# Performance work log

Measured on AMD Instinct MI355X. Metric: run time of the kernel, lower is better.

The kernel has to match this reference:

```python
import jax, jax.numpy as jnp
import numpy as np

DIMS, K_SIZE, V_SIZE = 256, 64, 64
B, T = 4, 4096


def setup_inputs() -> dict:
    key = jax.random.key(0)
    k1, k2, k3, k4 = jax.random.split(key, 4)
    # glorot-uniform-style init for the projection weights
    def glorot(k, fan_in, fan_out):
        lim = jnp.sqrt(6.0 / (fan_in + fan_out))
        return jax.random.uniform(k, (fan_in, fan_out), jnp.float32, -lim, lim)
    return {
        "inputs": jax.random.normal(k1, (B, T, DIMS), jnp.float32),
        "key_w": glorot(k2, DIMS, K_SIZE),
        "query_w": glorot(k3, DIMS, K_SIZE),
        "value_w": glorot(k4, DIMS, V_SIZE),
    }


def reference(inputs, key_w, query_w, value_w):
    # QKV projections: [B,T,D] @ [D,k] -> [B,T,k]
    keys = jnp.einsum('btd,dk->btk', inputs, key_w)
    queries = jnp.einsum('btd,dk->btk', inputs, query_w)
    values = jnp.einsum('btd,dv->btv', inputs, value_w)
    # full causal score matrix [B,T,T] (faithful to explicit triu mask)
    logits = jnp.einsum('bqk,bsk->bqs', queries, keys)
    q_idx = jnp.arange(logits.shape[1])[:, None]
    s_idx = jnp.arange(logits.shape[2])[None, :]
    causal = s_idx <= q_idx  # lower-triangular incl. diagonal
    sqrt_k = jnp.sqrt(jnp.asarray(key_w.shape[1], jnp.float32))
    masked = jnp.where(causal[None], logits, -jnp.inf)
    probs = jax.nn.softmax(masked / sqrt_k, axis=2)
    read = jnp.einsum('bqs,bsv->bqv', probs, values)
    return jnp.concatenate([inputs, read], axis=-1)  # [B,T,D+V]
```

## Files before the change

kernel.cpp:

```cpp
#include <hip/hip_runtime.h>

#define DIMS 256
#define HK 64
#define NB 4
#define NT 4096
#define BT (NB * NT)
#define SMAX 8

typedef unsigned short u16;
typedef unsigned int u32;

using f32x4  = __attribute__((ext_vector_type(4))) float;
using bf16x8 = __attribute__((ext_vector_type(8))) short;
using u32x2  = __attribute__((ext_vector_type(2))) u32;

__device__ __forceinline__ u16 f2bf(float f) {
    u32 u = __float_as_uint(f);
    u = (u + 0x7FFFu + ((u >> 16) & 1u)) >> 16;
    return (u16)u;
}
__device__ __forceinline__ u32 pack2(float a, float b) {
    return (u32)f2bf(a) | ((u32)f2bf(b) << 16);
}
__device__ __forceinline__ float bf2f(short h) {
    return __uint_as_float(((u32)(u16)h) << 16);
}
__device__ __forceinline__ bf16x8 ldb8(const u16* p) {
    return *reinterpret_cast<const bf16x8*>(p);
}
__device__ __forceinline__ u32 cvtpk(float a, float b) {
    u32 r;
    asm("v_cvt_pk_bf16_f32 %0, %1, %2" : "=v"(r) : "v"(a), "v"(b));
    return r;
}

__global__ __launch_bounds__(256) void prep_kernel(
    const float* __restrict__ x, const float* __restrict__ wk,
    const float* __restrict__ wq, const float* __restrict__ wv,
    float* __restrict__ out, u32* __restrict__ xb2, u16* __restrict__ Wt)
{
    const int stride = (int)(gridDim.x * blockDim.x);
    const int idx = (int)(blockIdx.x * blockDim.x + threadIdx.x);
    const f32x4* x4 = reinterpret_cast<const f32x4*>(x);
    f32x4* out4 = reinterpret_cast<f32x4*>(out);
    u32x2* xbv = reinterpret_cast<u32x2*>(xb2);

    for (int i = idx; i < BT * 64; i += stride) {
        f32x4 v = x4[i];
        out4[(size_t)(i >> 6) * 80 + (i & 63)] = v;
        u32x2 w;
        w.x = pack2(v[0], v[1]);
        w.y = pack2(v[2], v[3]);
        xbv[i] = w;
    }
    for (int i = idx; i < 12288; i += stride) {
        const int e0 = i * 4;
        const int m = e0 >> 14;
        const int r = e0 & 16383;
        const int col = r >> 8;
        const int k = r & 255;
        const float* w = (m == 0) ? wk : (m == 1) ? wq : wv;
        u32 w0 = pack2(w[(k + 0) * HK + col], w[(k + 1) * HK + col]);
        u32 w1 = pack2(w[(k + 2) * HK + col], w[(k + 3) * HK + col]);
        u32* p = reinterpret_cast<u32*>(Wt + e0);
        p[0] = w0; p[1] = w1;
    }
}

__global__ __launch_bounds__(64) void proj_kernel(
    const u16* __restrict__ xb, const u16* __restrict__ Wt,
    u16* __restrict__ Qb, u16* __restrict__ Kb, u16* __restrict__ Vt)
{
    const int l = (int)threadIdx.x;
    const int lo = l & 15;
    const int g = l >> 4;
    const int bid = (int)blockIdx.x;
    const int m = bid % 3;
    const int q0 = (bid / 3) * 16;

    bf16x8 a[8];
    const u16* xrow = xb + (size_t)(q0 + lo) * DIMS + g * 8;
    #pragma unroll
    for (int kf = 0; kf < 8; ++kf) a[kf] = ldb8(xrow + kf * 32);

    const u16* wb = Wt + m * (HK * DIMS);
    f32x4 acc[4];
    #pragma unroll
    for (int c = 0; c < 4; ++c) acc[c] = f32x4{0.f, 0.f, 0.f, 0.f};

    __builtin_amdgcn_s_setprio(1);
    #pragma unroll
    for (int c = 0; c < 4; ++c) {
        #pragma unroll
        for (int kf = 0; kf < 8; ++kf) {
            bf16x8 bf = ldb8(wb + (size_t)(16 * c + lo) * DIMS + kf * 32 + g * 8);
            acc[c] = __builtin_amdgcn_mfma_f32_16x16x32_bf16(a[kf], bf, acc[c], 0, 0, 0);
        }
    }
    __builtin_amdgcn_s_setprio(0);

    if (m == 2) {
        #pragma unroll
        for (int c = 0; c < 4; ++c)
            #pragma unroll
            for (int ii = 0; ii < 4; ++ii) {
                const int grow = q0 + 4 * g + ii;
                Vt[(size_t)((grow >> 12) * HK + 16 * c + lo) * NT + (grow & (NT - 1))] =
                    f2bf(acc[c][ii]);
            }
    } else {
        const float sc = (m == 1) ? 0.125f * 1.44269504f : 1.0f;
        u16* dst = (m == 1) ? Qb : Kb;
        #pragma unroll
        for (int c = 0; c < 4; ++c)
            #pragma unroll
            for (int ii = 0; ii < 4; ++ii)
                dst[(size_t)(q0 + 4 * g + ii) * HK + 16 * c + lo] = f2bf(acc[c][ii] * sc);
    }
}

template<bool MASK>
__device__ __forceinline__ void qk32(
    const u16* __restrict__ Kb_b, int s0, int q0,
    const bf16x8 (&qf)[2][2], float (&pls)[2], bf16x8 (&pa)[2],
    int lo, int g)
{
    bf16x8 kk[2][2];
    #pragma unroll
    for (int kh = 0; kh < 2; ++kh)
        #pragma unroll
        for (int kf = 0; kf < 2; ++kf)
            kk[kh][kf] = ldb8(Kb_b + (size_t)(s0 + 16 * kh + lo) * HK + kf * 32 + g * 8);

    const f32x4 c28 = f32x4{-28.f, -28.f, -28.f, -28.f};
    f32x4 sv[2][2];
    __builtin_amdgcn_s_setprio(1);
    #pragma unroll
    for (int rh = 0; rh < 2; ++rh)
        #pragma unroll
        for (int kh = 0; kh < 2; ++kh) {
            sv[rh][kh] = __builtin_amdgcn_mfma_f32_16x16x32_bf16(kk[kh][0], qf[rh][0], c28, 0, 0, 0);
            sv[rh][kh] = __builtin_amdgcn_mfma_f32_16x16x32_bf16(kk[kh][1], qf[rh][1], sv[rh][kh], 0, 0, 0);
        }
    __builtin_amdgcn_s_setprio(0);

    #pragma unroll
    for (int rh = 0; rh < 2; ++rh) {
        float p0[4], p1[4];
        #pragma unroll
        for (int ii = 0; ii < 4; ++ii) {
            float v0 = sv[rh][0][ii];
            float v1 = sv[rh][1][ii];
            if (MASK) {
                const int qr = q0 + 16 * rh + lo;
                if (s0 + 4 * g + ii > qr)      v0 = -1e30f;
                if (s0 + 16 + 4 * g + ii > qr) v1 = -1e30f;
            }
            p0[ii] = __builtin_amdgcn_exp2f(v0);
            p1[ii] = __builtin_amdgcn_exp2f(v1);
            pls[rh] += p0[ii] + p1[ii];
        }
        u32 a0 = cvtpk(p0[0], p0[1]), a1 = cvtpk(p0[2], p0[3]);
        u32 b0 = cvtpk(p1[0], p1[1]), b1 = cvtpk(p1[2], p1[3]);
        asm("v_permlane32_swap_b32 %0, %1" : "+v"(a0), "+v"(b0));
        asm("v_permlane16_swap_b32 %0, %1" : "+v"(a0), "+v"(b0));
        asm("v_permlane32_swap_b32 %0, %1" : "+v"(a1), "+v"(b1));
        asm("v_permlane16_swap_b32 %0, %1" : "+v"(a1), "+v"(b1));
        union { u32 w[4]; bf16x8 v; } u;
        u.w[0] = a0; u.w[1] = a1; u.w[2] = b0; u.w[3] = b1;
        pa[rh] = u.v;
    }
}

template<int NK, bool MASK>
__device__ __forceinline__ void body(
    const u16* __restrict__ Kb_b, const u16* __restrict__ Vb, int s0,
    const bf16x8 (&qf)[2][2], float (&pls)[2], f32x4 (&o)[2][4],
    int lo, int g, int q0)
{
    bf16x8 vf[NK][4];
    #pragma unroll
    for (int kf = 0; kf < NK; ++kf)
        #pragma unroll
        for (int c = 0; c < 4; ++c)
            vf[kf][c] = ldb8(Vb + (size_t)(16 * c + lo) * NT + s0 + kf * 32 + g * 8);

    #pragma unroll
    for (int t = 0; t < NK; ++t) {
        bf16x8 pa[2];
        qk32<MASK>(Kb_b, s0 + t * 32, q0, qf, pls, pa, lo, g);
        __builtin_amdgcn_s_setprio(1);
        #pragma unroll
        for (int rh = 0; rh < 2; ++rh)
            #pragma unroll
            for (int c = 0; c < 4; ++c)
                o[rh][c] = __builtin_amdgcn_mfma_f32_16x16x32_bf16(pa[rh], vf[t][c], o[rh][c], 0, 0, 0);
        __builtin_amdgcn_s_setprio(0);
    }
}

__global__ __launch_bounds__(64) void attn_kernel(
    const u16* __restrict__ Qb, const u16* __restrict__ Kb,
    const u16* __restrict__ Vt, u16* __restrict__ Opb, float* __restrict__ lp,
    const int S)
{
    const int l = (int)threadIdx.x;
    const int lo = l & 15;
    const int g = l >> 4;

    const int bid = (int)blockIdx.x;
    const int per = 4 * S;
    const int j = 127 - bid / per;
    const int r = bid % per;
    const int b = r / S;
    const int s = r % S;

    const int q0 = j * 32;
    const int nkv = j + 1;
    const int it0 = (s * nkv) / S;
    const int it1 = ((s + 1) * nkv) / S;

    const u16* Kb_b = Kb + (size_t)b * NT * HK;
    const u16* Vb = Vt + (size_t)b * HK * NT;

    bf16x8 qf[2][2];
    #pragma unroll
    for (int rh = 0; rh < 2; ++rh)
        #pragma unroll
        for (int kf = 0; kf < 2; ++kf)
            qf[rh][kf] = ldb8(Qb + (size_t)(b * NT + q0 + 16 * rh + lo) * HK + kf * 32 + g * 8);

    f32x4 o[2][4];
    float pls[2] = {0.f, 0.f};
    #pragma unroll
    for (int rh = 0; rh < 2; ++rh)
        #pragma unroll
        for (int c = 0; c < 4; ++c) o[rh][c] = f32x4{0.f, 0.f, 0.f, 0.f};

    int it = it0;
    const int itE = (s == S - 1) ? it1 - 1 : it1;
    for (; it + 1 < itE; it += 2)
        body<2, false>(Kb_b, Vb, it * 32, qf, pls, o, lo, g, q0);
    if (it < itE)
        body<1, false>(Kb_b, Vb, it * 32, qf, pls, o, lo, g, q0);
    if (s == S - 1)
        body<1, true>(Kb_b, Vb, (nkv - 1) * 32, qf, pls, o, lo, g, q0);

    const size_t rowbase = (size_t)s * BT + (size_t)b * NT + q0;
    #pragma unroll
    for (int rh = 0; rh < 2; ++rh) {
        #pragma unroll
        for (int c = 0; c < 4; ++c)
            #pragma unroll
            for (int ii = 0; ii < 4; ++ii)
                Opb[(rowbase + 16 * rh + 4 * g + ii) * HK + 16 * c + lo] = f2bf(o[rh][c][ii]);
        float sum = pls[rh];
        sum += __shfl_xor(sum, 16);
        sum += __shfl_xor(sum, 32);
        if (l < 16) lp[rowbase + 16 * rh + lo] = sum;
    }
}

__global__ __launch_bounds__(256) void merge_kernel(
    const u16* __restrict__ Opb, const float* __restrict__ lp,
    float* __restrict__ out, const int S)
{
    const int idx = (int)(blockIdx.x * 256 + threadIdx.x);
    const int row = idx >> 3;
    const int c8 = (idx & 7) * 8;

    float li = 0.f;
    for (int s = 0; s < S; ++s) li += lp[(size_t)s * BT + row];

    float acc[8];
    #pragma unroll
    for (int k = 0; k < 8; ++k) acc[k] = 0.f;
    for (int s = 0; s < S; ++s) {
        bf16x8 v = ldb8(Opb + ((size_t)s * BT + row) * HK + c8);
        #pragma unroll
        for (int k = 0; k < 8; ++k) acc[k] += bf2f(v[k]);
    }
    const float inv = 1.0f / li;
    f32x4 r0 = f32x4{acc[0] * inv, acc[1] * inv, acc[2] * inv, acc[3] * inv};
    f32x4 r1 = f32x4{acc[4] * inv, acc[5] * inv, acc[6] * inv, acc[7] * inv};
    f32x4* dst = reinterpret_cast<f32x4*>(out + (size_t)row * 320 + 256 + c8);
    dst[0] = r0;
    dst[1] = r1;
}

extern "C" void kernel_launch(void* const* d_in, const int* in_sizes, int n_in,
                              void* d_out, int out_size, void* d_ws, size_t ws_size,
                              hipStream_t stream) {
    (void)in_sizes; (void)n_in; (void)out_size;
    const float* x  = (const float*)d_in[0];
    const float* wk = (const float*)d_in[1];
    const float* wq = (const float*)d_in[2];
    const float* wv = (const float*)d_in[3];
    float* out = (float*)d_out;

    char* ws = (char*)d_ws;
    u16* Qb  = (u16*)(ws);
    u16* Kb  = (u16*)(ws + ((size_t)2  << 20));
    u16* Vt  = (u16*)(ws + ((size_t)4  << 20));
    u32* xb2 = (u32*)(ws + ((size_t)6  << 20));
    u16* xb  = (u16*)xb2;
    u16* Wt  = (u16*)(ws + ((size_t)14 << 20));
    float* lp = (float*)(ws + ((size_t)15 << 20));
    u16* Opb = (u16*)(ws + ((size_t)16 << 20));

    int S = SMAX;
    while (S > 1 && ((size_t)16 << 20) + (size_t)S * BT * HK * 2 > ws_size) S >>= 1;

    prep_kernel<<<1024, 256, 0, stream>>>(x, wk, wq, wv, out, xb2, Wt);
    proj_kernel<<<3072, 64, 0, stream>>>(xb, Wt, Qb, Kb, Vt);
    attn_kernel<<<128 * 4 * S, 64, 0, stream>>>(Qb, Kb, Vt, Opb, lp, S);
    merge_kernel<<<512, 256, 0, stream>>>(Opb, lp, out, S);
}
```

Baseline: 76.05 us.

## Fuse input conversion and passthrough copy into projection kernel

The bf16 conversion of the inputs and the copy of the inputs into the output move out of the prep kernel into the projection kernel, so the bf16 copy of x is no longer written to and read back from workspace. Each projection block now converts its 16 rows once and computes all three Q/K/V projections, where before a separate block handled each projection. The prep kernel now only transposes and converts the weights. In exchange the projection grid drops to a third as many blocks, each doing more serial work, which lowers parallelism in that stage.

```diff
diff --git a/kernel.cpp b/kernel.cpp
--- a/kernel.cpp
+++ b/kernel.cpp
@@ -5,14 +5,12 @@
 #define NB 4
 #define NT 4096
 #define BT (NB * NT)
-#define SMAX 8
 
 typedef unsigned short u16;
 typedef unsigned int u32;
 
 using f32x4  = __attribute__((ext_vector_type(4))) float;
 using bf16x8 = __attribute__((ext_vector_type(8))) short;
-using u32x2  = __attribute__((ext_vector_type(2))) u32;
 
 __device__ __forceinline__ u16 f2bf(float f) {
     u32 u = __float_as_uint(f);
@@ -33,89 +31,91 @@
     asm("v_cvt_pk_bf16_f32 %0, %1, %2" : "=v"(r) : "v"(a), "v"(b));
     return r;
 }
+__device__ __forceinline__ bf16x8 cvt8(const float* p) {
+    f32x4 a = *reinterpret_cast<const f32x4*>(p);
+    f32x4 b = *reinterpret_cast<const f32x4*>(p + 4);
+    union { u32 w[4]; bf16x8 v; } u;
+    u.w[0] = pack2(a[0], a[1]); u.w[1] = pack2(a[2], a[3]);
+    u.w[2] = pack2(b[0], b[1]); u.w[3] = pack2(b[2], b[3]);
+    return u.v;
+}
 
 __global__ __launch_bounds__(256) void prep_kernel(
-    const float* __restrict__ x, const float* __restrict__ wk,
-    const float* __restrict__ wq, const float* __restrict__ wv,
-    float* __restrict__ out, u32* __restrict__ xb2, u16* __restrict__ Wt)
-{
-    const int stride = (int)(gridDim.x * blockDim.x);
-    const int idx = (int)(blockIdx.x * blockDim.x + threadIdx.x);
-    const f32x4* x4 = reinterpret_cast<const f32x4*>(x);
-    f32x4* out4 = reinterpret_cast<f32x4*>(out);
-    u32x2* xbv = reinterpret_cast<u32x2*>(xb2);
-
-    for (int i = idx; i < BT * 64; i += stride) {
-        f32x4 v = x4[i];
-        out4[(size_t)(i >> 6) * 80 + (i & 63)] = v;
-        u32x2 w;
-        w.x = pack2(v[0], v[1]);
-        w.y = pack2(v[2], v[3]);
-        xbv[i] = w;
-    }
-    for (int i = idx; i < 12288; i += stride) {
-        const int e0 = i * 4;
-        const int m = e0 >> 14;
-        const int r = e0 & 16383;
-        const int col = r >> 8;
-        const int k = r & 255;
-        const float* w = (m == 0) ? wk : (m == 1) ? wq : wv;
-        u32 w0 = pack2(w[(k + 0) * HK + col], w[(k + 1) * HK + col]);
-        u32 w1 = pack2(w[(k + 2) * HK + col], w[(k + 3) * HK + col]);
-        u32* p = reinterpret_cast<u32*>(Wt + e0);
-        p[0] = w0; p[1] = w1;
-    }
+    const float* __restrict__ wk, const float* __restrict__ wq,
+    const float* __restrict__ wv, u16* __restrict__ Wt)
+{
+    const int i = (int)(blockIdx.x * 256 + threadIdx.x);
+    const int e0 = i * 4;
+    const int m = e0 >> 14;
+    const int r = e0 & 16383;
+    const int col = r >> 8;
+    const int k = r & 255;
+    const float* w = (m == 0) ? wk : (m == 1) ? wq : wv;
+    u32 w0 = pack2(w[(k + 0) * HK + col], w[(k + 1) * HK + col]);
+    u32 w1 = pack2(w[(k + 2) * HK + col], w[(k + 3) * HK + col]);
+    u32* p = reinterpret_cast<u32*>(Wt + e0);
+    p[0] = w0; p[1] = w1;
 }
 
 __global__ __launch_bounds__(64) void proj_kernel(
-    const u16* __restrict__ xb, const u16* __restrict__ Wt,
+    const float* __restrict__ x, const u16* __restrict__ Wt,
+    float* __restrict__ out,
     u16* __restrict__ Qb, u16* __restrict__ Kb, u16* __restrict__ Vt)
 {
     const int l = (int)threadIdx.x;
     const int lo = l & 15;
     const int g = l >> 4;
-    const int bid = (int)blockIdx.x;
-    const int m = bid % 3;
-    const int q0 = (bid / 3) * 16;
+    const int q0 = (int)blockIdx.x * 16;
+
+    const f32x4* x4 = reinterpret_cast<const f32x4*>(x);
+    f32x4* out4 = reinterpret_cast<f32x4*>(out);
+    #pragma unroll
+    for (int c = 0; c < 16; ++c) {
+        f32x4 v = x4[(size_t)(q0 + c) * 64 + l];
+        out4[(size_t)(q0 + c) * 80 + l] = v;
+    }
 
     bf16x8 a[8];
-    const u16* xrow = xb + (size_t)(q0 + lo) * DIMS + g * 8;
-    #pragma unroll
-    for (int kf = 0; kf < 8; ++kf) a[kf] = ldb8(xrow + kf * 32);
-
-    const u16* wb = Wt + m * (HK * DIMS);
-    f32x4 acc[4];
-    #pragma unroll
-    for (int c = 0; c < 4; ++c) acc[c] = f32x4{0.f, 0.f, 0.f, 0.f};
-
-    __builtin_amdgcn_s_setprio(1);
-    #pragma unroll
-    for (int c = 0; c < 4; ++c) {
-        #pragma unroll
-        for (int kf = 0; kf < 8; ++kf) {
-            bf16x8 bf = ldb8(wb + (size_t)(16 * c + lo) * DIMS + kf * 32 + g * 8);
-            acc[c] = __builtin_amdgcn_mfma_f32_16x16x32_bf16(a[kf], bf, acc[c], 0, 0, 0);
+    #pragma unroll
+    for (int kf = 0; kf < 8; ++kf)
+        a[kf] = cvt8(x + (size_t)(q0 + lo) * DIMS + kf * 32 + g * 8);
+
+    #pragma unroll
+    for (int m = 0; m < 3; ++m) {
+        const u16* wb = Wt + m * (HK * DIMS);
+        f32x4 acc[4];
+        #pragma unroll
+        for (int c = 0; c < 4; ++c) acc[c] = f32x4{0.f, 0.f, 0.f, 0.f};
+
+        __builtin_amdgcn_s_setprio(1);
+        #pragma unroll
+        for (int c = 0; c < 4; ++c) {
+            #pragma unroll
+            for (int kf = 0; kf < 8; ++kf) {
+                bf16x8 bf = ldb8(wb + (size_t)(16 * c + lo) * DIMS + kf * 32 + g * 8);
+                acc[c] = __builtin_amdgcn_mfma_f32_16x16x32_bf16(a[kf], bf, acc[c], 0, 0, 0);
+            }
         }
-    }
-    __builtin_amdgcn_s_setprio(0);
-
-    if (m == 2) {
-        #pragma unroll
-        for (int c = 0; c < 4; ++c)
-            #pragma unroll
-            for (int ii = 0; ii < 4; ++ii) {
-                const int grow = q0 + 4 * g + ii;
-                Vt[(size_t)((grow >> 12) * HK + 16 * c + lo) * NT + (grow & (NT - 1))] =
-                    f2bf(acc[c][ii]);
-            }
-    } else {
-        const float sc = (m == 1) ? 0.125f * 1.44269504f : 1.0f;
-        u16* dst = (m == 1) ? Qb : Kb;
-        #pragma unroll
-        for (int c = 0; c < 4; ++c)
-            #pragma unroll
-            for (int ii = 0; ii < 4; ++ii)
-                dst[(size_t)(q0 + 4 * g + ii) * HK + 16 * c + lo] = f2bf(acc[c][ii] * sc);
+        __builtin_amdgcn_s_setprio(0);
+
+        if (m == 2) {
+            #pragma unroll
+            for (int c = 0; c < 4; ++c)
+                #pragma unroll
+                for (int ii = 0; ii < 4; ++ii) {
+                    const int grow = q0 + 4 * g + ii;
+                    Vt[(size_t)((grow >> 12) * HK + 16 * c + lo) * NT + (grow & (NT - 1))] =
+                        f2bf(acc[c][ii]);
+                }
+        } else {
+            const float sc = (m == 1) ? 0.125f * 1.44269504f : 1.0f;
+            u16* dst = (m == 1) ? Qb : Kb;
+            #pragma unroll
+            for (int c = 0; c < 4; ++c)
+                #pragma unroll
+                for (int ii = 0; ii < 4; ++ii)
+                    dst[(size_t)(q0 + 4 * g + ii) * HK + 16 * c + lo] = f2bf(acc[c][ii] * sc);
+        }
     }
 }
 
@@ -300,19 +300,17 @@
 
     char* ws = (char*)d_ws;
     u16* Qb  = (u16*)(ws);
-    u16* Kb  = (u16*)(ws + ((size_t)2  << 20));
-    u16* Vt  = (u16*)(ws + ((size_t)4  << 20));
-    u32* xb2 = (u32*)(ws + ((size_t)6  << 20));
-    u16* xb  = (u16*)xb2;
-    u16* Wt  = (u16*)(ws + ((size_t)14 << 20));
-    float* lp = (float*)(ws + ((size_t)15 << 20));
-    u16* Opb = (u16*)(ws + ((size_t)16 << 20));
-
-    int S = SMAX;
-    while (S > 1 && ((size_t)16 << 20) + (size_t)S * BT * HK * 2 > ws_size) S >>= 1;
-
-    prep_kernel<<<1024, 256, 0, stream>>>(x, wk, wq, wv, out, xb2, Wt);
-    proj_kernel<<<3072, 64, 0, stream>>>(xb, Wt, Qb, Kb, Vt);
+    u16* Kb  = (u16*)(ws + ((size_t)2 << 20));
+    u16* Vt  = (u16*)(ws + ((size_t)4 << 20));
+    u16* Wt  = (u16*)(ws + ((size_t)6 << 20));
+    float* lp = (float*)(ws + ((size_t)6 << 20) + (128 << 10));
+    u16* Opb = (u16*)(ws + ((size_t)7 << 20));
+
+    int S = 8;
+    while (S > 1 && ((size_t)7 << 20) + (size_t)S * BT * HK * 2 > ws_size) S >>= 1;
+
+    prep_kernel<<<48, 256, 0, stream>>>(wk, wq, wv, Wt);
+    proj_kernel<<<BT / 16, 64, 0, stream>>>(x, Wt, out, Qb, Kb, Vt);
     attn_kernel<<<128 * 4 * S, 64, 0, stream>>>(Qb, Kb, Vt, Opb, lp, S);
     merge_kernel<<<512, 256, 0, stream>>>(Opb, lp, out, S);
 }
```

New measurement: 77.06 us. Within noise of the previous version (+1.3%).
